# Optimization experiments

Hardware: AMD Instinct MI355X
Metric: run time of the kernel (lower is better)

Reference implementation:

```python
import jax, jax.numpy as jnp
import numpy as np

C_IN = 1.0
C_OUT = 1.0
N_NODES = 10000
D_IN = 256
D_OUT = 256
N_EDGES = 320000
MIN_NORM = 1e-15
BALL_EPS = 4e-3  # float32 boundary eps used by HGCN PoincareBall


def _norm(x):
    return jnp.maximum(jnp.linalg.norm(x, axis=-1, keepdims=True), MIN_NORM)


def _artanh(x):
    x = jnp.clip(x, -1.0 + 1e-7, 1.0 - 1e-7)
    return 0.5 * (jnp.log1p(x) - jnp.log1p(-x))


def proj(x, c):
    norm = _norm(x)
    maxnorm = (1.0 - BALL_EPS) / jnp.sqrt(c)
    return jnp.where(norm > maxnorm, x / norm * maxnorm, x)


def expmap0(u, c):
    sc = jnp.sqrt(c)
    un = _norm(u)
    return jnp.tanh(sc * un) * u / (sc * un)


def logmap0(p, c):
    sc = jnp.sqrt(c)
    pn = _norm(p)
    return _artanh(sc * pn) * p / (sc * pn)


def mobius_add(x, y, c):
    x2 = jnp.sum(x * x, -1, keepdims=True)
    y2 = jnp.sum(y * y, -1, keepdims=True)
    xy = jnp.sum(x * y, -1, keepdims=True)
    num = (1 + 2 * c * xy + c * y2) * x + (1 - c * x2) * y
    denom = 1 + 2 * c * xy + c * c * x2 * y2
    return num / jnp.maximum(denom, MIN_NORM)


def mobius_matvec(m, x, c):
    sc = jnp.sqrt(c)
    xn = _norm(x)
    mx = x @ m.T  # [N, D_out]
    mxn = _norm(mx)
    res = jnp.tanh(mxn / xn * _artanh(sc * xn)) * mx / (mxn * sc)
    cond = jnp.all(mx == 0, axis=-1, keepdims=True)
    return jnp.where(cond, jnp.zeros_like(res), res)


def setup_inputs() -> dict:
    key = jax.random.key(0)
    k = jax.random.split(key, 6)
    x = jax.random.normal(k[0], (N_NODES, D_IN), jnp.float32) * 0.05
    x = proj(x, C_IN)  # valid points on the Poincare ball
    weight = jax.random.normal(k[1], (D_OUT, D_IN), jnp.float32) * (1.0 / np.sqrt(D_IN))
    bias = jax.random.normal(k[2], (D_OUT,), jnp.float32) * 0.01
    adj_val = jax.random.uniform(k[3], (N_EDGES,), jnp.float32) * (1.0 / 32.0)
    adj_row = jnp.sort(jax.random.randint(k[4], (N_EDGES,), 0, N_NODES, jnp.int32))
    adj_col = jax.random.randint(k[5], (N_EDGES,), 0, N_NODES, jnp.int32)
    return {"x": x, "weight": weight, "bias": bias, "adj_val": adj_val,
            "adj_row": adj_row, "adj_col": adj_col}


def reference(x, weight, bias, adj_val, adj_row, adj_col):
    # --- HypLinear: mobius matvec + hyperbolic bias ---
    h = proj(mobius_matvec(weight, x, C_IN), C_IN)
    hyp_bias = proj(expmap0(bias[None, :], C_IN), C_IN)  # proj_tan0 is identity
    h = proj(mobius_add(h, hyp_bias, C_IN), C_IN)
    # --- HypAgg: tangent-space sparse aggregation ---
    x_t = logmap0(h, C_IN)  # [N, D_out]
    msgs = adj_val[:, None] * x_t[adj_col]  # [E, D_out]
    support_t = jax.ops.segment_sum(msgs, adj_row, num_segments=N_NODES)
    h = proj(expmap0(support_t, C_IN), C_IN)
    # --- HypAct: act in tangent space, remap with c_out ---
    xt = jax.nn.relu(logmap0(h, C_IN))
    return proj(expmap0(xt, C_OUT), C_OUT)
```

## Files before the change

### kernel.cpp

```cpp
#include <hip/hip_runtime.h>
#include <math.h>

#define D 256
#define MAXNORM (1.0f - 4e-3f)
#define MIN_NORM 1e-15f

typedef _Float16 v8h __attribute__((ext_vector_type(8)));
typedef _Float16 h4  __attribute__((ext_vector_type(4)));
typedef float    v4f __attribute__((ext_vector_type(4)));

__device__ __forceinline__ float wave_reduce_sum(float v) {
    #pragma unroll
    for (int m = 32; m >= 1; m >>= 1) v += __shfl_xor(v, m, 64);
    return v;
}

__device__ __forceinline__ float dot4(const float4& a, const float4& b) {
    return a.x * b.x + a.y * b.y + a.z * b.z + a.w * b.w;
}

__device__ __forceinline__ float artanh_clip(float x) {
    x = fminf(fmaxf(x, -1.0f + 1e-7f), 1.0f - 1e-7f);
    return 0.5f * (log1pf(x) - log1pf(-x));
}

__global__ __launch_bounds__(256) void prep_kernel(
    const float* __restrict__ bias, const float* __restrict__ W,
    const int* __restrict__ rows,
    float* __restrict__ HB, _Float16* __restrict__ Wh,
    int* __restrict__ rowptr, int N, int E)
{
    const int b = blockIdx.x, t = threadIdx.x;
    const int e = b * 256 + t;

    if (e < E) {
        int r1 = rows[e];
        if (e == 0) {
            for (int r = 0; r <= r1; ++r) rowptr[r] = 0;
        } else {
            int r0 = rows[e - 1];
            for (int r = r0 + 1; r <= r1; ++r) rowptr[r] = e;
        }
        if (e == E - 1) {
            for (int r = r1 + 1; r <= N; ++r) rowptr[r] = E;
        }
    }

    if (b < 64) {
        int i = b * 256 + t;
        float4 v = ((const float4*)W)[i];
        h4 o; o[0] = (_Float16)v.x; o[1] = (_Float16)v.y;
        o[2] = (_Float16)v.z; o[3] = (_Float16)v.w;
        *(h4*)(Wh + 4 * (size_t)i) = o;
    }

    if (b == 64 && t < 64) {
        int l = t;
        float4 v = *(const float4*)(bias + 4 * l);
        float bn = fmaxf(sqrtf(wave_reduce_sum(dot4(v, v))), MIN_NORM);
        float f = tanhf(bn) / bn;
        float4 h = make_float4(v.x * f, v.y * f, v.z * f, v.w * f);
        float hn = fmaxf(sqrtf(wave_reduce_sum(dot4(h, h))), MIN_NORM);
        float s = (hn > MAXNORM) ? (MAXNORM / hn) : 1.0f;
        h.x *= s; h.y *= s; h.z *= s; h.w *= s;
        *(float4*)(HB + 4 * l) = h;
        float y2 = wave_reduce_sum(dot4(h, h));
        if (l == 0) HB[D] = y2;
    }
}

#define AS16 264

__global__ __launch_bounds__(256) void gemmrow_kernel(
    const float* __restrict__ X, const _Float16* __restrict__ Wh,
    const float* __restrict__ HB, _Float16* __restrict__ XT, int N)
{
    __shared__ _Float16 As[16 * AS16];
    __shared__ float xnsq[16];
    __shared__ float part_s[16][4];
    __shared__ float part_d[16][4];
    __shared__ float Arow[16], Brow[16];

    const int t = threadIdx.x;
    const int r0 = blockIdx.x * 16;

    {
        const int r = t >> 4, q2 = t & 15;
        const int grow = r0 + r;
        float ss = 0.0f;
        #pragma unroll
        for (int j = 0; j < 4; ++j) {
            const int fi = q2 + j * 16;
            float4 v = make_float4(0.f, 0.f, 0.f, 0.f);
            if (grow < N) v = ((const float4*)X)[(size_t)grow * 64 + fi];
            ss += dot4(v, v);
            h4 hv; hv[0] = (_Float16)v.x; hv[1] = (_Float16)v.y;
            hv[2] = (_Float16)v.z; hv[3] = (_Float16)v.w;
            *(h4*)&As[r * AS16 + fi * 4] = hv;
        }
        ss += __shfl_xor(ss, 1, 64);
        ss += __shfl_xor(ss, 2, 64);
        ss += __shfl_xor(ss, 4, 64);
        ss += __shfl_xor(ss, 8, 64);
        if (q2 == 0) xnsq[r] = ss;
    }
    __syncthreads();

    const int w  = t >> 6;
    const int l  = t & 63;
    const int lm = l & 15;
    const int q  = l >> 4;

    v4f acc[4];
    #pragma unroll
    for (int ct = 0; ct < 4; ++ct)
        #pragma unroll
        for (int i = 0; i < 4; ++i) acc[ct][i] = 0.0f;

    const _Float16* WhB = Wh + (size_t)(64 * w + lm) * 256 + q * 8;

    #pragma unroll
    for (int kc = 0; kc < 8; ++kc) {
        v8h a = *(const v8h*)&As[lm * AS16 + kc * 32 + q * 8];
        #pragma unroll
        for (int ct = 0; ct < 4; ++ct) {
            v8h bfr = *(const v8h*)(WhB + (size_t)ct * 16 * 256 + kc * 32);
            acc[ct] = __builtin_amdgcn_mfma_f32_16x16x32_f16(a, bfr, acc[ct], 0, 0, 0);
        }
    }

    float yv[4];
    #pragma unroll
    for (int ct = 0; ct < 4; ++ct) yv[ct] = HB[64 * w + ct * 16 + lm];

    {
        float s_[4], d_[4];
        #pragma unroll
        for (int i = 0; i < 4; ++i) {
            float s = 0.f, d = 0.f;
            #pragma unroll
            for (int ct = 0; ct < 4; ++ct) {
                float v = acc[ct][i];
                s = fmaf(v, v, s);
                d = fmaf(v, yv[ct], d);
            }
            #pragma unroll
            for (int m = 1; m <= 8; m <<= 1) {
                s += __shfl_xor(s, m, 64);
                d += __shfl_xor(d, m, 64);
            }
            s_[i] = s; d_[i] = d;
        }
        if (lm == 0) {
            #pragma unroll
            for (int i = 0; i < 4; ++i) {
                part_s[q * 4 + i][w] = s_[i];
                part_d[q * 4 + i][w] = d_[i];
            }
        }
    }
    __syncthreads();

    if (t < 16) {
        float mx2 = part_s[t][0] + part_s[t][1] + part_s[t][2] + part_s[t][3];
        float mxy = part_d[t][0] + part_d[t][1] + part_d[t][2] + part_d[t][3];
        float y2  = HB[D];
        float xn  = fmaxf(sqrtf(xnsq[t]), MIN_NORM);
        float mxn = fmaxf(sqrtf(mx2), MIN_NORM);
        float r  = (mxn / xn) * artanh_clip(xn);
        float th = tanhf(r);
        float f  = th / mxn;
        float hn = fmaxf(th, MIN_NORM);
        float s  = (hn > MAXNORM) ? (MAXNORM / hn) : 1.0f;
        float fs = f * s;
        float x2 = th * th * s * s;
        float xy  = fs * mxy;
        float ch  = 1.0f + 2.0f * xy + y2;
        float cy  = 1.0f - x2;
        float inv = 1.0f / fmaxf(1.0f + 2.0f * xy + x2 * y2, MIN_NORM);
        float alpha = ch * fs * inv;
        float beta  = cy * inv;
        float gss = alpha * alpha * mx2 + 2.0f * alpha * beta * mxy + beta * beta * y2;
        float gn  = fmaxf(sqrtf(gss), MIN_NORM);
        float s2  = (gn > MAXNORM) ? (MAXNORM / gn) : 1.0f;
        float pn  = fmaxf(gn * s2, MIN_NORM);
        float lf  = artanh_clip(pn) / pn;
        Arow[t] = lf * s2 * alpha;
        Brow[t] = lf * s2 * beta;
    }
    __syncthreads();

    #pragma unroll
    for (int i = 0; i < 4; ++i) {
        const int rr = q * 4 + i;
        const int row = r0 + rr;
        if (row < N) {
            float A = Arow[rr], B = Brow[rr];
            #pragma unroll
            for (int ct = 0; ct < 4; ++ct) {
                float v = fmaf(A, acc[ct][i], B * yv[ct]);
                XT[(size_t)row * 256 + 64 * w + ct * 16 + lm] = (_Float16)v;
            }
        }
    }
}

__global__ __launch_bounds__(256) void agg_kernel(
    const int* __restrict__ rowptr, const int* __restrict__ cols,
    const float* __restrict__ vals, const _Float16* __restrict__ XT,
    float* __restrict__ OUT, int N)
{
    int node = (int)((blockIdx.x * (size_t)blockDim.x + threadIdx.x) >> 6);
    int l = threadIdx.x & 63;
    if (node >= N) return;

    int start = rowptr[node];
    int end   = rowptr[node + 1];

    const h4* xt4 = (const h4*)XT;
    float4 acc = make_float4(0.f, 0.f, 0.f, 0.f);

    for (int base = start; base < end; base += 64) {
        int idx = base + l;
        bool ok = idx < end;
        int   myc = ok ? cols[idx] : 0;
        float myv = ok ? vals[idx] : 0.0f;
        int cnt = min(64, end - base);
        int cnt8 = (cnt + 7) & ~7;

        for (int j = 0; j < cnt8; j += 8) {
            int   c[8];
            float v[8];
            #pragma unroll
            for (int u = 0; u < 8; ++u) {
                c[u] = __shfl(myc, j + u, 64);
                v[u] = __shfl(myv, j + u, 64);
            }
            h4 m[8];
            #pragma unroll
            for (int u = 0; u < 8; ++u)
                m[u] = xt4[(size_t)c[u] * 64 + l];
            #pragma unroll
            for (int u = 0; u < 8; ++u) {
                acc.x = fmaf(v[u], (float)m[u][0], acc.x);
                acc.y = fmaf(v[u], (float)m[u][1], acc.y);
                acc.z = fmaf(v[u], (float)m[u][2], acc.z);
                acc.w = fmaf(v[u], (float)m[u][3], acc.w);
            }
        }
    }

    float un = fmaxf(sqrtf(wave_reduce_sum(dot4(acc, acc))), MIN_NORM);
    float f = tanhf(un) / un;
    float4 h = make_float4(acc.x * f, acc.y * f, acc.z * f, acc.w * f);
    float hn = fmaxf(sqrtf(wave_reduce_sum(dot4(h, h))), MIN_NORM);
    float s = (hn > MAXNORM) ? (MAXNORM / hn) : 1.0f;
    h.x *= s; h.y *= s; h.z *= s; h.w *= s;
    float pn = fmaxf(hn * s, MIN_NORM);
    float lf = artanh_clip(pn) / pn;
    float4 tt = make_float4(fmaxf(h.x * lf, 0.f), fmaxf(h.y * lf, 0.f),
                            fmaxf(h.z * lf, 0.f), fmaxf(h.w * lf, 0.f));
    float un2 = fmaxf(sqrtf(wave_reduce_sum(dot4(tt, tt))), MIN_NORM);
    float f2 = tanhf(un2) / un2;
    float4 o = make_float4(tt.x * f2, tt.y * f2, tt.z * f2, tt.w * f2);
    float on = fmaxf(sqrtf(wave_reduce_sum(dot4(o, o))), MIN_NORM);
    float s2 = (on > MAXNORM) ? (MAXNORM / on) : 1.0f;
    o.x *= s2; o.y *= s2; o.z *= s2; o.w *= s2;

    *(float4*)(OUT + (size_t)node * D + 4 * l) = o;
}

extern "C" void kernel_launch(void* const* d_in, const int* in_sizes, int n_in,
                              void* d_out, int out_size, void* d_ws, size_t ws_size,
                              hipStream_t stream) {
    const float* X    = (const float*)d_in[0];
    const float* W    = (const float*)d_in[1];
    const float* bias = (const float*)d_in[2];
    const float* vals = (const float*)d_in[3];
    const int*   rows = (const int*)d_in[4];
    const int*   cols = (const int*)d_in[5];
    float* OUT = (float*)d_out;

    const int N = in_sizes[0] / D;
    const int E = in_sizes[3];

    int*      rowptr = (int*)d_ws;
    float*    HB = (float*)d_ws + 10240;
    _Float16* Wh = (_Float16*)((float*)d_ws + 10240 + 512);
    _Float16* XT = (_Float16*)((float*)d_ws + 10240 + 512 + 32768);

    prep_kernel<<<(E + 255) / 256, 256, 0, stream>>>(bias, W, rows, HB, Wh, rowptr, N, E);
    gemmrow_kernel<<<(N + 15) / 16, 256, 0, stream>>>(X, Wh, HB, XT, N);
    int wave_blocks = (N + 3) / 4;
    agg_kernel<<<wave_blocks, 256, 0, stream>>>(rowptr, cols, vals, XT, OUT, N);
}
```

Before: 109.8 us.

## Use 16-byte gathers with 4 edges per pass in SpMM aggregation kernel

```diff
diff --git a/kernel.cpp b/kernel.cpp
--- a/kernel.cpp
+++ b/kernel.cpp
@@ -217,8 +217,13 @@
     int start = rowptr[node];
     int end   = rowptr[node + 1];
 
-    const h4* xt4 = (const h4*)XT;
-    float4 acc = make_float4(0.f, 0.f, 0.f, 0.f);
+    const int sub = l >> 4;
+    const int ch  = l & 15;
+
+    const v8h* xt8 = (const v8h*)XT;
+
+    float accA[8] = {0.f,0.f,0.f,0.f,0.f,0.f,0.f,0.f};
+    float accB[8] = {0.f,0.f,0.f,0.f,0.f,0.f,0.f,0.f};
 
     for (int base = start; base < end; base += 64) {
         int idx = base + l;
@@ -226,48 +231,84 @@
         int   myc = ok ? cols[idx] : 0;
         float myv = ok ? vals[idx] : 0.0f;
         int cnt = min(64, end - base);
-        int cnt8 = (cnt + 7) & ~7;
-
-        for (int j = 0; j < cnt8; j += 8) {
+        int cnt32 = (cnt + 31) & ~31;
+
+        for (int j = 0; j < cnt32; j += 32) {
             int   c[8];
             float v[8];
             #pragma unroll
             for (int u = 0; u < 8; ++u) {
-                c[u] = __shfl(myc, j + u, 64);
-                v[u] = __shfl(myv, j + u, 64);
-            }
-            h4 m[8];
+                c[u] = __shfl(myc, j + 4 * u + sub, 64);
+                v[u] = __shfl(myv, j + 4 * u + sub, 64);
+            }
+            v8h m[8];
             #pragma unroll
             for (int u = 0; u < 8; ++u)
-                m[u] = xt4[(size_t)c[u] * 64 + l];
+                m[u] = xt8[(size_t)c[u] * 32 + ch];
             #pragma unroll
             for (int u = 0; u < 8; ++u) {
-                acc.x = fmaf(v[u], (float)m[u][0], acc.x);
-                acc.y = fmaf(v[u], (float)m[u][1], acc.y);
-                acc.z = fmaf(v[u], (float)m[u][2], acc.z);
-                acc.w = fmaf(v[u], (float)m[u][3], acc.w);
-            }
-        }
-    }
-
-    float un = fmaxf(sqrtf(wave_reduce_sum(dot4(acc, acc))), MIN_NORM);
-    float f = tanhf(un) / un;
-    float4 h = make_float4(acc.x * f, acc.y * f, acc.z * f, acc.w * f);
-    float hn = fmaxf(sqrtf(wave_reduce_sum(dot4(h, h))), MIN_NORM);
-    float s = (hn > MAXNORM) ? (MAXNORM / hn) : 1.0f;
-    h.x *= s; h.y *= s; h.z *= s; h.w *= s;
+                #pragma unroll
+                for (int k = 0; k < 8; ++k)
+                    accA[k] = fmaf(v[u], (float)m[u][k], accA[k]);
+            }
+            #pragma unroll
+            for (int u = 0; u < 8; ++u)
+                m[u] = xt8[(size_t)c[u] * 32 + 16 + ch];
+            #pragma unroll
+            for (int u = 0; u < 8; ++u) {
+                #pragma unroll
+                for (int k = 0; k < 8; ++k)
+                    accB[k] = fmaf(v[u], (float)m[u][k], accB[k]);
+            }
+        }
+    }
+
+    #pragma unroll
+    for (int k = 0; k < 8; ++k) {
+        accA[k] += __shfl_xor(accA[k], 16, 64);
+        accA[k] += __shfl_xor(accA[k], 32, 64);
+        accB[k] += __shfl_xor(accB[k], 16, 64);
+        accB[k] += __shfl_xor(accB[k], 32, 64);
+    }
+
+    float ss = 0.f;
+    #pragma unroll
+    for (int k = 0; k < 8; ++k) ss += accA[k]*accA[k] + accB[k]*accB[k];
+    #pragma unroll
+    for (int mk = 1; mk <= 8; mk <<= 1) ss += __shfl_xor(ss, mk, 64);
+
+    float un = fmaxf(sqrtf(ss), MIN_NORM);
+    float f  = tanhf(un) / un;
+    float hn = f * un;
+    float s  = (hn > MAXNORM) ? (MAXNORM / hn) : 1.0f;
     float pn = fmaxf(hn * s, MIN_NORM);
     float lf = artanh_clip(pn) / pn;
-    float4 tt = make_float4(fmaxf(h.x * lf, 0.f), fmaxf(h.y * lf, 0.f),
-                            fmaxf(h.z * lf, 0.f), fmaxf(h.w * lf, 0.f));
-    float un2 = fmaxf(sqrtf(wave_reduce_sum(dot4(tt, tt))), MIN_NORM);
-    float f2 = tanhf(un2) / un2;
-    float4 o = make_float4(tt.x * f2, tt.y * f2, tt.z * f2, tt.w * f2);
-    float on = fmaxf(sqrtf(wave_reduce_sum(dot4(o, o))), MIN_NORM);
-    float s2 = (on > MAXNORM) ? (MAXNORM / on) : 1.0f;
-    o.x *= s2; o.y *= s2; o.z *= s2; o.w *= s2;
-
-    *(float4*)(OUT + (size_t)node * D + 4 * l) = o;
+    float g  = f * s * lf;
+    float tA[8], tB[8];
+    float ss2 = 0.f;
+    #pragma unroll
+    for (int k = 0; k < 8; ++k) {
+        tA[k] = fmaxf(accA[k] * g, 0.f);
+        tB[k] = fmaxf(accB[k] * g, 0.f);
+        ss2 += tA[k]*tA[k] + tB[k]*tB[k];
+    }
+    #pragma unroll
+    for (int mk = 1; mk <= 8; mk <<= 1) ss2 += __shfl_xor(ss2, mk, 64);
+
+    float un2 = fmaxf(sqrtf(ss2), MIN_NORM);
+    float f2  = tanhf(un2) / un2;
+    float on  = f2 * un2;
+    float s2  = (on > MAXNORM) ? (MAXNORM / on) : 1.0f;
+    float fo  = f2 * s2;
+
+    const int q = sub;
+    int off = (q >> 1) * 128 + ch * 8 + (q & 1) * 4;
+    float4 wv;
+    if (q == 0)      wv = make_float4(tA[0]*fo, tA[1]*fo, tA[2]*fo, tA[3]*fo);
+    else if (q == 1) wv = make_float4(tA[4]*fo, tA[5]*fo, tA[6]*fo, tA[7]*fo);
+    else if (q == 2) wv = make_float4(tB[0]*fo, tB[1]*fo, tB[2]*fo, tB[3]*fo);
+    else             wv = make_float4(tB[4]*fo, tB[5]*fo, tB[6]*fo, tB[7]*fo);
+    *(float4*)(OUT + (size_t)node * D + off) = wv;
 }
 
 extern "C" void kernel_launch(void* const* d_in, const int* in_sizes, int n_in,
```

Result: slower. 117.8 us (+7.3%).

## Quantize tangent features to per-row int8 for the sparse aggregation gather

Applied to the files above, without the earlier changes.

```diff
diff --git a/kernel.cpp b/kernel.cpp
--- a/kernel.cpp
+++ b/kernel.cpp
@@ -73,13 +73,17 @@
 
 __global__ __launch_bounds__(256) void gemmrow_kernel(
     const float* __restrict__ X, const _Float16* __restrict__ Wh,
-    const float* __restrict__ HB, _Float16* __restrict__ XT, int N)
+    const float* __restrict__ HB, unsigned char* __restrict__ XT8,
+    float* __restrict__ SCg, int N)
 {
     __shared__ _Float16 As[16 * AS16];
     __shared__ float xnsq[16];
     __shared__ float part_s[16][4];
     __shared__ float part_d[16][4];
     __shared__ float Arow[16], Brow[16];
+    __shared__ float pmax[16][4];
+    __shared__ float Srow[16];
+    __shared__ unsigned char stage[16 * 256];
 
     const int t = threadIdx.x;
     const int r0 = blockIdx.x * 16;
@@ -190,24 +194,60 @@
     }
     __syncthreads();
 
+    {
+        float vmax[4];
+        #pragma unroll
+        for (int i = 0; i < 4; ++i) {
+            const int rr = q * 4 + i;
+            float A = Arow[rr], B = Brow[rr];
+            float m = 0.f;
+            #pragma unroll
+            for (int ct = 0; ct < 4; ++ct)
+                m = fmaxf(m, fabsf(fmaf(A, acc[ct][i], B * yv[ct])));
+            #pragma unroll
+            for (int mk = 1; mk <= 8; mk <<= 1)
+                m = fmaxf(m, __shfl_xor(m, mk, 64));
+            vmax[i] = m;
+        }
+        if (lm == 0) {
+            #pragma unroll
+            for (int i = 0; i < 4; ++i) pmax[q * 4 + i][w] = vmax[i];
+        }
+    }
+    __syncthreads();
+    if (t < 16) {
+        float rm = fmaxf(fmaxf(pmax[t][0], pmax[t][1]),
+                         fmaxf(pmax[t][2], pmax[t][3]));
+        Srow[t] = 127.0f / fmaxf(rm, 1e-30f);
+        if (r0 + t < N) SCg[r0 + t] = rm * (1.0f / 127.0f);
+    }
+    __syncthreads();
+
     #pragma unroll
     for (int i = 0; i < 4; ++i) {
         const int rr = q * 4 + i;
-        const int row = r0 + rr;
-        if (row < N) {
-            float A = Arow[rr], B = Brow[rr];
-            #pragma unroll
-            for (int ct = 0; ct < 4; ++ct) {
-                float v = fmaf(A, acc[ct][i], B * yv[ct]);
-                XT[(size_t)row * 256 + 64 * w + ct * 16 + lm] = (_Float16)v;
-            }
-        }
+        float A = Arow[rr], B = Brow[rr], S = Srow[rr];
+        #pragma unroll
+        for (int ct = 0; ct < 4; ++ct) {
+            float v = fmaf(A, acc[ct][i], B * yv[ct]) * S;
+            v = fminf(fmaxf(v, -127.0f), 127.0f);
+            int qi = (int)rintf(v) + 128;
+            stage[rr * 256 + 64 * w + ct * 16 + lm] = (unsigned char)qi;
+        }
+    }
+    __syncthreads();
+    {
+        const int rr2 = t >> 4, seg = t & 15;
+        if (r0 + rr2 < N)
+            *(uint4*)(XT8 + (size_t)(r0 + rr2) * 256 + seg * 16) =
+                *(const uint4*)&stage[rr2 * 256 + seg * 16];
     }
 }
 
 __global__ __launch_bounds__(256) void agg_kernel(
     const int* __restrict__ rowptr, const int* __restrict__ cols,
-    const float* __restrict__ vals, const _Float16* __restrict__ XT,
+    const float* __restrict__ vals, const float* __restrict__ SCg,
+    const unsigned int* __restrict__ XT8u,
     float* __restrict__ OUT, int N)
 {
     int node = (int)((blockIdx.x * (size_t)blockDim.x + threadIdx.x) >> 6);
@@ -217,38 +257,46 @@
     int start = rowptr[node];
     int end   = rowptr[node + 1];
 
-    const h4* xt4 = (const h4*)XT;
     float4 acc = make_float4(0.f, 0.f, 0.f, 0.f);
+    float sw = 0.0f;
 
     for (int base = start; base < end; base += 64) {
         int idx = base + l;
         bool ok = idx < end;
         int   myc = ok ? cols[idx] : 0;
-        float myv = ok ? vals[idx] : 0.0f;
+        float myv = ok ? vals[idx] * SCg[myc] : 0.0f;
         int cnt = min(64, end - base);
-        int cnt8 = (cnt + 7) & ~7;
-
-        for (int j = 0; j < cnt8; j += 8) {
-            int   c[8];
-            float v[8];
-            #pragma unroll
-            for (int u = 0; u < 8; ++u) {
-                c[u] = __shfl(myc, j + u, 64);
-                v[u] = __shfl(myv, j + u, 64);
-            }
-            h4 m[8];
-            #pragma unroll
-            for (int u = 0; u < 8; ++u)
-                m[u] = xt4[(size_t)c[u] * 64 + l];
-            #pragma unroll
-            for (int u = 0; u < 8; ++u) {
-                acc.x = fmaf(v[u], (float)m[u][0], acc.x);
-                acc.y = fmaf(v[u], (float)m[u][1], acc.y);
-                acc.z = fmaf(v[u], (float)m[u][2], acc.z);
-                acc.w = fmaf(v[u], (float)m[u][3], acc.w);
-            }
-        }
-    }
+        int cnt16 = (cnt + 15) & ~15;
+
+        for (int j = 0; j < cnt16; j += 16) {
+            int   cc[16];
+            float ww[16];
+            #pragma unroll
+            for (int u = 0; u < 16; ++u) {
+                cc[u] = __shfl(myc, j + u, 64);
+                ww[u] = __shfl(myv, j + u, 64);
+            }
+            unsigned int mw[16];
+            #pragma unroll
+            for (int u = 0; u < 16; ++u)
+                mw[u] = XT8u[(size_t)cc[u] * 64 + l];
+            #pragma unroll
+            for (int u = 0; u < 16; ++u) {
+                float f0 = (float)( mw[u]        & 0xffu);
+                float f1 = (float)((mw[u] >> 8)  & 0xffu);
+                float f2 = (float)((mw[u] >> 16) & 0xffu);
+                float f3 = (float)( mw[u] >> 24);
+                acc.x = fmaf(ww[u], f0, acc.x);
+                acc.y = fmaf(ww[u], f1, acc.y);
+                acc.z = fmaf(ww[u], f2, acc.z);
+                acc.w = fmaf(ww[u], f3, acc.w);
+                sw += ww[u];
+            }
+        }
+    }
+
+    float corr = 128.0f * sw;
+    acc.x -= corr; acc.y -= corr; acc.z -= corr; acc.w -= corr;
 
     float un = fmaxf(sqrtf(wave_reduce_sum(dot4(acc, acc))), MIN_NORM);
     float f = tanhf(un) / un;
@@ -284,13 +332,15 @@
     const int N = in_sizes[0] / D;
     const int E = in_sizes[3];
 
-    int*      rowptr = (int*)d_ws;
-    float*    HB = (float*)d_ws + 10240;
-    _Float16* Wh = (_Float16*)((float*)d_ws + 10240 + 512);
-    _Float16* XT = (_Float16*)((float*)d_ws + 10240 + 512 + 32768);
+    int*           rowptr = (int*)d_ws;
+    float*         HB  = (float*)d_ws + 10240;
+    _Float16*      Wh  = (_Float16*)((float*)d_ws + 10240 + 512);
+    float*         SCg = (float*)d_ws + 10240 + 512 + 32768;
+    unsigned char* XT8 = (unsigned char*)((float*)d_ws + 10240 + 512 + 32768 + 10240);
 
     prep_kernel<<<(E + 255) / 256, 256, 0, stream>>>(bias, W, rows, HB, Wh, rowptr, N, E);
-    gemmrow_kernel<<<(N + 15) / 16, 256, 0, stream>>>(X, Wh, HB, XT, N);
+    gemmrow_kernel<<<(N + 15) / 16, 256, 0, stream>>>(X, Wh, HB, XT8, SCg, N);
     int wave_blocks = (N + 3) / 4;
-    agg_kernel<<<wave_blocks, 256, 0, stream>>>(rowptr, cols, vals, XT, OUT, N);
-}
+    agg_kernel<<<wave_blocks, 256, 0, stream>>>(rowptr, cols, vals, SCg,
+                                                (const unsigned int*)XT8, OUT, N);
+}
```

Result: no change. 108.3 us (-1.3%).
